# Kernel optimization log

Measured on AMD Instinct MI355X. Metric: run time of the kernel, lower is better.

Reference implementation:

```python
import jax, jax.numpy as jnp
import numpy as np

B, N, C, D = 32, 4096, 16, 256

def setup_inputs() -> dict:
    key = jax.random.key(0)
    k1, k2 = jax.random.split(key)
    r_tensor = jax.random.uniform(k1, (B, N, C), dtype=jnp.float32)
    v_tensor = jax.random.normal(k2, (B, N, D), dtype=jnp.float32)
    return {"r_tensor": r_tensor, "v_tensor": v_tensor}

def reference(r_tensor, v_tensor):
    n = r_tensor.shape[1]
    mask_belong = r_tensor >= 0.5  # (B,N,C)
    # mean over N of v[:, :, None, :] * mask[..., None]  ==  mask^T @ v / N, no (B,N,C,D) intermediate
    interest_category_mean = jnp.einsum(
        'bnc,bnd->bcd', mask_belong.astype(v_tensor.dtype), v_tensor) / n  # (B,C,D)
    mask_all_below = jnp.logical_not(mask_belong).all(axis=2)  # (B,N)
    interest_special_mean = jnp.einsum(
        'bn,bnd->bd', mask_all_below.astype(v_tensor.dtype), v_tensor) / n  # (B,D)
    v_fusion = jnp.concatenate(
        [interest_category_mean, interest_special_mean[:, None, :]], axis=1)  # (B,C+1,D)
    v_fusion = jnp.where(jnp.isnan(v_fusion), jnp.zeros((), v_fusion.dtype), v_fusion)
    return v_fusion
```

## Files before the change

kernel.cpp:

```cpp
#include <hip/hip_runtime.h>

#define B_ 32
#define N_ 4096
#define C_ 16
#define D_ 256
#define NSPLIT 16
#define ROWS (N_ / NSPLIT)

__global__ __launch_bounds__(256, 4)
void tensor_fusion_kernel(const float* __restrict__ r,
                          const float* __restrict__ v,
                          float* __restrict__ out) {
    const int b     = blockIdx.x >> 4;
    const int chunk = blockIdx.x & (NSPLIT - 1);
    const int tid   = threadIdx.x;
    const int wave  = tid >> 6;
    const int lane  = tid & 63;
    const int d4    = lane << 2;

    const float* __restrict__ rb = r + (size_t)b * N_ * C_;
    const float* __restrict__ vb = v + (size_t)b * N_ * D_;

    float4 acc[17];
#pragma unroll
    for (int c = 0; c < 17; ++c) acc[c] = make_float4(0.f, 0.f, 0.f, 0.f);

    const int n0 = chunk * ROWS;

    int n = n0 + wave;
    float  rv = (lane < C_) ? rb[(size_t)n * C_ + lane] : 0.0f;
    float4 v4 = *(const float4*)(vb + (size_t)n * D_ + d4);

    for (int i = 0; i < ROWS; i += 4) {
        const int npf = n + ((i + 4 < ROWS) ? 4 : 0);
        const float  rvn = (lane < C_) ? rb[(size_t)npf * C_ + lane] : 0.0f;
        const float4 v4n = *(const float4*)(vb + (size_t)npf * D_ + d4);

        const unsigned long long bal = __ballot(rv >= 0.5f);
        const unsigned mask = (unsigned)bal & 0xFFFFu;
#pragma unroll
        for (int c = 0; c < 16; ++c) {
            if (mask & (1u << c)) {
                acc[c].x += v4.x; acc[c].y += v4.y;
                acc[c].z += v4.z; acc[c].w += v4.w;
            }
        }
        if (mask == 0u) {
            acc[16].x += v4.x; acc[16].y += v4.y;
            acc[16].z += v4.z; acc[16].w += v4.w;
        }
        rv = rvn; v4 = v4n; n = npf;
    }

    __shared__ float lds[17 * D_];
#pragma unroll
    for (int i = tid; i < 17 * D_; i += 256) lds[i] = 0.0f;
    __syncthreads();
    for (int w = 0; w < 4; ++w) {
        if (wave == w) {
#pragma unroll
            for (int c = 0; c < 17; ++c) {
                lds[c * D_ + d4 + 0] += acc[c].x;
                lds[c * D_ + d4 + 1] += acc[c].y;
                lds[c * D_ + d4 + 2] += acc[c].z;
                lds[c * D_ + d4 + 3] += acc[c].w;
            }
        }
        __syncthreads();
    }

    const float scale = 1.0f / (float)N_;
    float* __restrict__ ob = out + (size_t)b * 17 * D_;
#pragma unroll
    for (int c = 0; c < 17; ++c) {
        atomicAdd(&ob[c * D_ + tid], lds[c * D_ + tid] * scale);
    }
}

extern "C" void kernel_launch(void* const* d_in, const int* in_sizes, int n_in,
                              void* d_out, int out_size, void* d_ws, size_t ws_size,
                              hipStream_t stream) {
    const float* r = (const float*)d_in[0];
    const float* v = (const float*)d_in[1];
    float* out = (float*)d_out;

    hipMemsetAsync(out, 0, (size_t)out_size * sizeof(float), stream);

    dim3 grid(B_ * NSPLIT);
    tensor_fusion_kernel<<<grid, 256, 0, stream>>>(r, v, out);
}
```

Baseline: 214.3 us.

## Split N across more blocks, process two rows per wave step, atomically accumulate special rows

Raises the grid from 16 to 64 chunks per batch and gives each wave a contiguous run of rows, reading two rows per iteration with a single ballot over 32 lanes of r. The special (all-below) row is no longer kept in registers; it is added straight to global output with atomics, which cuts accumulator registers from 17 to 16 float4. The LDS reduction is seeded by wave 0 storing directly, with float4 accesses, so no zeroing pass is needed. The aim is more parallelism and occupancy on a bandwidth-bound reduction. The costs are four times as many final atomics to the output and extra per-row global atomics for special rows, although with uniform r those rows are rare (about 2^-16 per row).

```diff
diff --git a/kernel.cpp b/kernel.cpp
--- a/kernel.cpp
+++ b/kernel.cpp
@@ -4,14 +4,15 @@
 #define N_ 4096
 #define C_ 16
 #define D_ 256
-#define NSPLIT 16
+#define NSPLIT 64
 #define ROWS (N_ / NSPLIT)
+#define RPW  (ROWS / 4)
 
 __global__ __launch_bounds__(256, 4)
 void tensor_fusion_kernel(const float* __restrict__ r,
                           const float* __restrict__ v,
                           float* __restrict__ out) {
-    const int b     = blockIdx.x >> 4;
+    const int b     = blockIdx.x >> 6;
     const int chunk = blockIdx.x & (NSPLIT - 1);
     const int tid   = threadIdx.x;
     const int wave  = tid >> 6;
@@ -19,61 +20,81 @@
     const int d4    = lane << 2;
 
     const float* __restrict__ rb = r + (size_t)b * N_ * C_;
-    const float* __restrict__ vb = v + (size_t)b * N_ * D_;
+    const float* __restrict__ vp = v + (size_t)b * N_ * D_;
+    const float scale = 1.0f / (float)N_;
+    float* __restrict__ ob = out + (size_t)b * 17 * D_;
 
-    float4 acc[17];
+    float4 acc[16];
 #pragma unroll
-    for (int c = 0; c < 17; ++c) acc[c] = make_float4(0.f, 0.f, 0.f, 0.f);
+    for (int c = 0; c < 16; ++c) acc[c] = make_float4(0.f, 0.f, 0.f, 0.f);
 
-    const int n0 = chunk * ROWS;
+    const int base = chunk * ROWS + wave * RPW;
 
-    int n = n0 + wave;
-    float  rv = (lane < C_) ? rb[(size_t)n * C_ + lane] : 0.0f;
-    float4 v4 = *(const float4*)(vb + (size_t)n * D_ + d4);
+    float  rv  = (lane < 32) ? rb[(size_t)base * C_ + lane] : 0.0f;
+    float4 va  = *(const float4*)(vp + (size_t)base * D_ + d4);
+    float4 vb4 = *(const float4*)(vp + (size_t)(base + 1) * D_ + d4);
 
-    for (int i = 0; i < ROWS; i += 4) {
-        const int npf = n + ((i + 4 < ROWS) ? 4 : 0);
-        const float  rvn = (lane < C_) ? rb[(size_t)npf * C_ + lane] : 0.0f;
-        const float4 v4n = *(const float4*)(vb + (size_t)npf * D_ + d4);
+    for (int i = 0; i < RPW; i += 2) {
+        const int nn = base + ((i + 2 < RPW) ? i + 2 : i);
+        const float  rv_n = (lane < 32) ? rb[(size_t)nn * C_ + lane] : 0.0f;
+        const float4 va_n = *(const float4*)(vp + (size_t)nn * D_ + d4);
+        const float4 vb_n = *(const float4*)(vp + (size_t)(nn + 1) * D_ + d4);
 
-        const unsigned long long bal = __ballot(rv >= 0.5f);
-        const unsigned mask = (unsigned)bal & 0xFFFFu;
+        const unsigned bal   = (unsigned)__ballot(rv >= 0.5f);
+        const unsigned maskA = bal & 0xFFFFu;
+        const unsigned maskB = (bal >> 16) & 0xFFFFu;
 #pragma unroll
         for (int c = 0; c < 16; ++c) {
-            if (mask & (1u << c)) {
-                acc[c].x += v4.x; acc[c].y += v4.y;
-                acc[c].z += v4.z; acc[c].w += v4.w;
+            if (maskA & (1u << c)) {
+                acc[c].x += va.x; acc[c].y += va.y;
+                acc[c].z += va.z; acc[c].w += va.w;
             }
         }
-        if (mask == 0u) {
-            acc[16].x += v4.x; acc[16].y += v4.y;
-            acc[16].z += v4.z; acc[16].w += v4.w;
+#pragma unroll
+        for (int c = 0; c < 16; ++c) {
+            if (maskB & (1u << c)) {
+                acc[c].x += vb4.x; acc[c].y += vb4.y;
+                acc[c].z += vb4.z; acc[c].w += vb4.w;
+            }
         }
-        rv = rvn; v4 = v4n; n = npf;
+        if (maskA == 0u) {
+            atomicAdd(&ob[16 * D_ + d4 + 0], va.x * scale);
+            atomicAdd(&ob[16 * D_ + d4 + 1], va.y * scale);
+            atomicAdd(&ob[16 * D_ + d4 + 2], va.z * scale);
+            atomicAdd(&ob[16 * D_ + d4 + 3], va.w * scale);
+        }
+        if (maskB == 0u) {
+            atomicAdd(&ob[16 * D_ + d4 + 0], vb4.x * scale);
+            atomicAdd(&ob[16 * D_ + d4 + 1], vb4.y * scale);
+            atomicAdd(&ob[16 * D_ + d4 + 2], vb4.z * scale);
+            atomicAdd(&ob[16 * D_ + d4 + 3], vb4.w * scale);
+        }
+        rv = rv_n; va = va_n; vb4 = vb_n;
     }
 
-    __shared__ float lds[17 * D_];
+    __shared__ float4 lds4[16 * 64];
+    if (wave == 0) {
 #pragma unroll
-    for (int i = tid; i < 17 * D_; i += 256) lds[i] = 0.0f;
+        for (int c = 0; c < 16; ++c) lds4[c * 64 + lane] = acc[c];
+    }
     __syncthreads();
-    for (int w = 0; w < 4; ++w) {
+    for (int w = 1; w < 4; ++w) {
         if (wave == w) {
 #pragma unroll
-            for (int c = 0; c < 17; ++c) {
-                lds[c * D_ + d4 + 0] += acc[c].x;
-                lds[c * D_ + d4 + 1] += acc[c].y;
-                lds[c * D_ + d4 + 2] += acc[c].z;
-                lds[c * D_ + d4 + 3] += acc[c].w;
+            for (int c = 0; c < 16; ++c) {
+                float4 t = lds4[c * 64 + lane];
+                t.x += acc[c].x; t.y += acc[c].y;
+                t.z += acc[c].z; t.w += acc[c].w;
+                lds4[c * 64 + lane] = t;
             }
         }
         __syncthreads();
     }
 
-    const float scale = 1.0f / (float)N_;
-    float* __restrict__ ob = out + (size_t)b * 17 * D_;
+    const float* lf = (const float*)lds4;
 #pragma unroll
-    for (int c = 0; c < 17; ++c) {
-        atomicAdd(&ob[c * D_ + tid], lds[c * D_ + tid] * scale);
+    for (int c = 0; c < 16; ++c) {
+        atomicAdd(&ob[c * D_ + tid], lf[c * 256 + tid] * scale);
     }
 }
 
```

Result: no change. 214.7 us (+0.2%).
